# Optimization experiments

Hardware: AMD Instinct MI355X
Metric: run time of the kernel (lower is better)

The kernel has to match this reference:

```python
import jax, jax.numpy as jnp
import numpy as np

N = 8192
TEMP = 0.5
EPS = 1e-12


def _normalize(z):
    # F.normalize(z, p=2, dim=1): x / max(||x||, eps)
    n = jnp.sqrt(jnp.sum(z * z, axis=1, keepdims=True))
    return z / jnp.maximum(n, EPS)


def _gcn(edge_index, edge_weight, x, w, b):
    # torch.sparse.mm(adj, x @ w): out[row] += adj[row, col] * support[col]
    support = x @ w
    msg = support[edge_index[1]] * edge_weight[:, None]
    return jax.ops.segment_sum(msg, edge_index[0], num_segments=N) + b


def _encoder(edge_index, edge_weight, feat, w_l1a, b_l1a, w_l1b, b_l1b, w_g1, b_g1, w_g2, b_g2):
    x = jax.nn.relu(feat @ w_l1a + b_l1a) @ w_l1b + b_l1b  # [N, 32]
    h = jax.nn.relu(_gcn(edge_index, edge_weight, x, w_g1, b_g1))  # [N, hid]
    return _gcn(edge_index, edge_weight, h, w_g2, b_g2)  # [N, act_fn]


def _proj(h, w_fc1, b_fc1, w_fc2, b_fc2):
    return jax.nn.elu(h @ w_fc1 + b_fc1) @ w_fc2 + b_fc2


def _loss(z1, z2):
    z1n = _normalize(z1)
    z2n = _normalize(z2)
    refl = jnp.exp((z1n @ z1n.T) / TEMP)      # [N, N]
    between = jnp.exp((z1n @ z2n.T) / TEMP)   # [N, N]
    denom = refl.sum(1) + between.sum(1) - jnp.diagonal(refl)
    return -jnp.log(jnp.diagonal(between) / denom)


def setup_inputs() -> dict:
    key = jax.random.key(0)
    ks = jax.random.split(key, 20)
    E = 262144
    in_dim, hid_dim, act_fn, out_dim = 512, 256, 128, 64

    def kaiming(k, shape):
        fan_in = shape[0]
        bound = np.sqrt(6.0 / fan_in)
        return jax.random.uniform(k, shape, jnp.float32, -bound, bound)

    return {
        "feat1": jax.random.normal(ks[0], (N, in_dim), jnp.float32),
        "feat2": jax.random.normal(ks[1], (N, in_dim), jnp.float32),
        "edge_index1": jax.random.randint(ks[2], (2, E), 0, N, jnp.int32),
        "edge_weight1": jax.random.uniform(ks[3], (E,), jnp.float32),
        "edge_index2": jax.random.randint(ks[4], (2, E), 0, N, jnp.int32),
        "edge_weight2": jax.random.uniform(ks[5], (E,), jnp.float32),
        "w_l1a": kaiming(ks[6], (in_dim, 64)),
        "b_l1a": jnp.zeros((64,), jnp.float32),
        "w_l1b": kaiming(ks[7], (64, 32)),
        "b_l1b": jnp.zeros((32,), jnp.float32),
        "w_g1": kaiming(ks[8], (32, hid_dim)),
        "b_g1": jnp.zeros((hid_dim,), jnp.float32),
        "w_g2": kaiming(ks[9], (hid_dim, act_fn)),
        "b_g2": jnp.zeros((act_fn,), jnp.float32),
        "w_fc1": kaiming(ks[10], (act_fn, out_dim)),
        "b_fc1": jnp.zeros((out_dim,), jnp.float32),
        "w_fc2": kaiming(ks[11], (out_dim, act_fn)),
        "b_fc2": jnp.zeros((act_fn,), jnp.float32),
    }


def reference(feat1, feat2, edge_index1, edge_weight1, edge_index2, edge_weight2,
              w_l1a, b_l1a, w_l1b, b_l1b, w_g1, b_g1, w_g2, b_g2,
              w_fc1, b_fc1, w_fc2, b_fc2):
    h1 = _encoder(edge_index1, edge_weight1, feat1, w_l1a, b_l1a, w_l1b, b_l1b, w_g1, b_g1, w_g2, b_g2)
    h2 = _encoder(edge_index2, edge_weight2, feat2, w_l1a, b_l1a, w_l1b, b_l1b, w_g1, b_g1, w_g2, b_g2)
    z1 = _proj(h1, w_fc1, b_fc1, w_fc2, b_fc2)
    z2 = _proj(h2, w_fc1, b_fc1, w_fc2, b_fc2)
    l1 = _loss(z1, z2)
    l2 = _loss(z2, z1)
    return ((l1 + l2) * 0.5).mean()
```

## Files before the change

kernel.cpp:

```cpp
#include <hip/hip_runtime.h>
#include <hip/hip_bf16.h>
#include <math.h>


#define NROWS 8192
#define MROWS 16384
#define NEDGE 262144

typedef __attribute__((ext_vector_type(8))) short bf16x8;
typedef __attribute__((ext_vector_type(4))) float f32x4;
typedef __attribute__((ext_vector_type(2))) float f32x2;
typedef long long i64;

__device__ __forceinline__ short f2bf(float f){
  union { float f; unsigned u; } cv; cv.f = f;
  unsigned u = cv.u;
  unsigned r = (u + 0x7fffu + ((u >> 16) & 1u)) >> 16;
  return (short)r;
}
__device__ __forceinline__ f32x4 mfma16(bf16x8 a, bf16x8 b, f32x4 c){
  return __builtin_amdgcn_mfma_f32_16x16x32_bf16(a, b, c, 0, 0, 0);
}
__device__ __forceinline__ float fexp2(float x){
#if __has_builtin(__builtin_amdgcn_exp2f)
  return __builtin_amdgcn_exp2f(x);
#else
  return exp2f(x);
#endif
}

__device__ unsigned char f2e4m3_sw(float f){
  float a = fabsf(f);
  unsigned s = (__float_as_uint(f)>>24)&0x80u;
  if (!(a>0.f)) return (unsigned char)s;
  if (a>448.f) a=448.f;
  int e; frexpf(a,&e);
  int eff=e-1;
  unsigned code;
  if (eff<-6){
    float q=rintf(a*512.f);
    code=(unsigned)q; if(code>7)code=7;
  } else {
    float q=rintf(a*exp2f((float)(3-eff)));
    unsigned mant=(unsigned)q;
    if(mant>=16){mant=8;eff++;}
    if(eff>8) return (unsigned char)(s|0x7e);
    code=((unsigned)(eff+7)<<3)|(mant-8);
  }
  return (unsigned char)(s|code);
}
__device__ __forceinline__ unsigned short pack2fp8(float a, float b){
#if __has_builtin(__builtin_amdgcn_cvt_pk_fp8_f32)
  int v = __builtin_amdgcn_cvt_pk_fp8_f32(a, b, 0, false);
  return (unsigned short)(v & 0xffff);
#else
  return (unsigned short)((unsigned)f2e4m3_sw(a) | ((unsigned)f2e4m3_sw(b)<<8));
#endif
}

struct WtArgs {
  const float* src[6];
  short* dst[6];
  int K[6], N[6];
  int off[7];
  int nwt;
};
__global__ void setup_k(WtArgs a, const int* __restrict__ ei1, const int* __restrict__ ei2,
                        int* __restrict__ deg1, int* __restrict__ deg2){
  int b = blockIdx.x;
  if (b < a.nwt){
    int i = b*256 + threadIdx.x;
    if (i >= a.off[6]) return;
    int s = 0;
    #pragma unroll
    for (int j=1;j<6;j++) if (i >= a.off[j]) s=j;
    int l = i - a.off[s];
    int K=a.K[s], N=a.N[s];
    int k=l/N, n=l-k*N;
    a.dst[s][(long)n*K+k] = f2bf(a.src[s][l]);
  } else {
    int hb = b - a.nwt;
    const int* ei = (hb < NEDGE/256) ? ei1 : ei2;
    int* deg = (hb < NEDGE/256) ? deg1 : deg2;
    int e = (hb % (NEDGE/256))*256 + threadIdx.x;
    atomicAdd(&deg[ei[e]], 1);
  }
}

__global__ __launch_bounds__(256) void mlp12_k(const float* __restrict__ F0, const float* __restrict__ F1,
                                               const short* __restrict__ Wa, const float* __restrict__ ba,
                                               const short* __restrict__ Wb, const float* __restrict__ bb,
                                               short* __restrict__ xb){
  __shared__ short As[32*520];
  __shared__ short a1s[32*72];
  const int tid = threadIdx.x;
  const int m0 = blockIdx.x*32;
  const float* F = (m0 < NROWS) ? (F0 + (long)m0*512) : (F1 + (long)(m0-NROWS)*512);
  {
    float4 st[16];
    #pragma unroll
    for (int i=0;i<16;i++) st[i] = *(const float4*)(F + (long)(i*256+tid)*4);
    #pragma unroll
    for (int i=0;i<16;i++){
      int idx = i*256+tid, row = idx>>7, c4 = idx&127;
      unsigned lo = (unsigned)(unsigned short)f2bf(st[i].x) | ((unsigned)(unsigned short)f2bf(st[i].y)<<16);
      unsigned hi = (unsigned)(unsigned short)f2bf(st[i].z) | ((unsigned)(unsigned short)f2bf(st[i].w)<<16);
      uint2 o = {lo, hi};
      *(uint2*)&As[row*520 + c4*4] = o;
    }
  }
  __syncthreads();
  const int wave = tid>>6, lane = tid&63, quad = lane>>4, cl = lane&15;
  f32x4 zero = {0.f,0.f,0.f,0.f};
  {
    const int wno = wave*16;
    f32x4 acc[2] = {zero, zero};
    #pragma unroll
    for (int kc=0;kc<16;kc++){
      const int ko = kc*32 + quad*8;
      bf16x8 a0 = *(const bf16x8*)&As[(cl)*520 + ko];
      bf16x8 a1 = *(const bf16x8*)&As[(16+cl)*520 + ko];
      bf16x8 b = *(const bf16x8*)(Wa + (long)(wno + cl)*512 + ko);
      acc[0] = mfma16(a0, b, acc[0]);
      acc[1] = mfma16(a1, b, acc[1]);
    }
    int col = wno + cl;
    float bv = ba[col];
    #pragma unroll
    for (int mt=0;mt<2;mt++)
      #pragma unroll
      for (int r=0;r<4;r++)
        a1s[(mt*16 + quad*4 + r)*72 + col] = f2bf(fmaxf(acc[mt][r] + bv, 0.f));
  }
  __syncthreads();
  if (wave < 2){
    f32x4 acc2[2] = {zero, zero};
    #pragma unroll
    for (int kc=0;kc<2;kc++){
      const int ko = kc*32 + quad*8;
      bf16x8 a = *(const bf16x8*)&a1s[(wave*16+cl)*72 + ko];
      #pragma unroll
      for (int nt=0;nt<2;nt++){
        bf16x8 b = *(const bf16x8*)(Wb + (long)(nt*16 + cl)*64 + ko);
        acc2[nt] = mfma16(a, b, acc2[nt]);
      }
    }
    #pragma unroll
    for (int nt=0;nt<2;nt++){
      int col = nt*16 + cl;
      float bv = bb[col];
      #pragma unroll
      for (int r=0;r<4;r++)
        xb[(long)(m0 + wave*16 + quad*4 + r)*32 + col] = f2bf(acc2[nt][r] + bv);
    }
  }
}

__global__ void scan2_k(const int* __restrict__ deg1, int* __restrict__ rs1, int* __restrict__ cur1,
                        const int* __restrict__ deg2, int* __restrict__ rs2, int* __restrict__ cur2){
  const int* deg = blockIdx.x ? deg2 : deg1;
  int* rowstart = blockIdx.x ? rs2 : rs1;
  int* cursor = blockIdx.x ? cur2 : cur1;
  __shared__ int csum[256];
  int t = threadIdx.x;
  int loc[32];
  int s = 0;
  for (int j=0;j<32;j++){ int d = deg[t*32+j]; loc[j] = s; s += d; }
  int v = s;
  csum[t] = v;
  __syncthreads();
  for (int st=1; st<256; st<<=1){
    int o = (t >= st) ? csum[t-st] : 0;
    __syncthreads();
    v += o;
    csum[t] = v;
    __syncthreads();
  }
  int base = v - s;
  for (int j=0;j<32;j++){ int w = base + loc[j]; rowstart[t*32+j]=w; cursor[t*32+j]=w; }
  if (t==255) rowstart[NROWS] = v;
}
__global__ void fill2_k(const int* __restrict__ ei1, const float* __restrict__ w1, int* __restrict__ cur1,
                        int* __restrict__ ecol1, float* __restrict__ ew1,
                        const int* __restrict__ ei2, const float* __restrict__ w2, int* __restrict__ cur2,
                        int* __restrict__ ecol2, float* __restrict__ ew2){
  int b = blockIdx.x;
  bool g2 = (b >= NEDGE/256);
  const int* ei = g2 ? ei2 : ei1;
  const float* w = g2 ? w2 : w1;
  int* cursor = g2 ? cur2 : cur1;
  int* ecol = g2 ? ecol2 : ecol1;
  float* ew = g2 ? ew2 : ew1;
  int e = (b % (NEDGE/256))*256 + threadIdx.x;
  int r = ei[e];
  int p = atomicAdd(&cursor[r], 1);
  ecol[p] = ei[NEDGE + e];
  ew[p] = w[e];
}

__device__ __forceinline__ void acc8(float* acc, int4 v, float f){
  const unsigned* u = (const unsigned*)&v;
  #pragma unroll
  for (int i=0;i<4;i++){
    union{unsigned x; float y;} lo, hi;
    lo.x = u[i] << 16;
    hi.x = u[i] & 0xffff0000u;
    acc[2*i]   = fmaf(f, lo.y, acc[2*i]);
    acc[2*i+1] = fmaf(f, hi.y, acc[2*i+1]);
  }
}
template<int C>
__device__ __forceinline__ void gather_row(float* acc, const short* sb,
                                           const int* ec, const float* w, int s, int e){
  int k = s;
  for (; k+16 <= e; k+=16){
    int c[16]; float f[16]; int4 v[16];
    #pragma unroll
    for (int u=0;u<16;u++){ c[u]=ec[k+u]; f[u]=w[k+u]; }
    #pragma unroll
    for (int u=0;u<16;u++) v[u] = *(const int4*)(sb + (long)c[u]*C);
    #pragma unroll
    for (int u=0;u<16;u++) acc8(acc, v[u], f[u]);
  }
  for (; k+4 <= e; k+=4){
    int c0=ec[k],c1=ec[k+1],c2=ec[k+2],c3=ec[k+3];
    float f0=w[k],f1=w[k+1],f2=w[k+2],f3=w[k+3];
    int4 v0 = *(const int4*)(sb + (long)c0*C);
    int4 v1 = *(const int4*)(sb + (long)c1*C);
    int4 v2 = *(const int4*)(sb + (long)c2*C);
    int4 v3 = *(const int4*)(sb + (long)c3*C);
    acc8(acc,v0,f0); acc8(acc,v1,f1); acc8(acc,v2,f2); acc8(acc,v3,f3);
  }
  for (; k < e; k++){
    int4 v0 = *(const int4*)(sb + (long)ec[k]*C);
    acc8(acc,v0,w[k]);
  }
}

template<int C, bool RELU, bool HASB>
__global__ __launch_bounds__(256) void gather_k(const short* __restrict__ sup,
    const int* __restrict__ rs1, const int* __restrict__ ec1, const float* __restrict__ w1,
    const int* __restrict__ rs2, const int* __restrict__ ec2, const float* __restrict__ w2,
    const float* __restrict__ bias, short* __restrict__ out){
  constexpr int G = C/8;
  const int g = threadIdx.x % G;
  const int sub = threadIdx.x / G;
  const int row = blockIdx.x*(256/G) + sub;
  const int* rs; const int* ec; const float* w; int soff, lr;
  if (row < NROWS){ rs=rs1; ec=ec1; w=w1; soff=0; lr=row; }
  else            { rs=rs2; ec=ec2; w=w2; soff=NROWS; lr=row-NROWS; }
  const short* sb = sup + (long)soff*C + g*8;
  float acc[8];
  #pragma unroll
  for (int j=0;j<8;j++) acc[j] = HASB ? bias[g*8+j] : 0.f;
  gather_row<C>(acc, sb, ec, w, rs[lr], rs[lr+1]);
  int4 ov;
  unsigned* ou = (unsigned*)&ov;
  #pragma unroll
  for (int i=0;i<4;i++){
    float a0 = acc[2*i], a1 = acc[2*i+1];
    if (RELU){ a0 = fmaxf(a0,0.f); a1 = fmaxf(a1,0.f); }
    ou[i] = (unsigned)(unsigned short)f2bf(a0) | ((unsigned)(unsigned short)f2bf(a1)<<16);
  }
  *(int4*)(out + (long)row*C + g*8) = ov;
}

__global__ __launch_bounds__(256) void gg_k(const short* __restrict__ xb,
    const int* __restrict__ rs1, const int* __restrict__ ec1, const float* __restrict__ w1,
    const int* __restrict__ rs2, const int* __restrict__ ec2, const float* __restrict__ w2,
    const short* __restrict__ Wg1, const float* __restrict__ bg1,
    const short* __restrict__ Wg2, short* __restrict__ s2){
  __shared__ short axs[64*40];
  __shared__ short hbs[64*264];
  const int tid = threadIdx.x;
  const int m0 = blockIdx.x*64;
  {
    const int g = tid & 3, sub = tid >> 2;
    const int row = m0 + sub;
    const int* rs; const int* ec; const float* w; int soff, lr;
    if (row < NROWS){ rs=rs1; ec=ec1; w=w1; soff=0; lr=row; }
    else            { rs=rs2; ec=ec2; w=w2; soff=NROWS; lr=row-NROWS; }
    const short* sb = xb + (long)soff*32 + g*8;
    float acc[8];
    #pragma unroll
    for (int j=0;j<8;j++) acc[j] = 0.f;
    gather_row<32>(acc, sb, ec, w, rs[lr], rs[lr+1]);
    int4 ov;
    unsigned* ou = (unsigned*)&ov;
    #pragma unroll
    for (int i=0;i<4;i++)
      ou[i] = (unsigned)(unsigned short)f2bf(acc[2*i]) | ((unsigned)(unsigned short)f2bf(acc[2*i+1])<<16);
    *(int4*)&axs[sub*40 + g*8] = ov;
  }
  __syncthreads();
  const int wave = tid>>6, lane = tid&63, quad = lane>>4, cl = lane&15;
  f32x4 zero = {0.f,0.f,0.f,0.f};
  {
    const int wno = wave*64;
    f32x4 acc[4][4];
    #pragma unroll
    for (int i=0;i<4;i++)
      #pragma unroll
      for (int j=0;j<4;j++) acc[i][j]=zero;
    const int ko = quad*8;
    bf16x8 a[4], b[4];
    #pragma unroll
    for (int mt=0;mt<4;mt++)
      a[mt] = *(const bf16x8*)&axs[(mt*16+cl)*40 + ko];
    #pragma unroll
    for (int nt=0;nt<4;nt++)
      b[nt] = *(const bf16x8*)(Wg1 + (long)(wno + nt*16 + cl)*32 + ko);
    #pragma unroll
    for (int mt=0;mt<4;mt++)
      #pragma unroll
      for (int nt=0;nt<4;nt++)
        acc[mt][nt] = mfma16(a[mt], b[nt], acc[mt][nt]);
    #pragma unroll
    for (int nt=0;nt<4;nt++){
      int col = wno + nt*16 + cl;
      float bv = bg1[col];
      #pragma unroll
      for (int mt=0;mt<4;mt++)
        #pragma unroll
        for (int r=0;r<4;r++)
          hbs[(mt*16 + quad*4 + r)*264 + col] = f2bf(fmaxf(acc[mt][nt][r] + bv, 0.f));
    }
  }
  __syncthreads();
  {
    const int wno = wave*32;
    f32x4 acc[4][2];
    #pragma unroll
    for (int i=0;i<4;i++){ acc[i][0]=zero; acc[i][1]=zero; }
    #pragma unroll
    for (int kc=0;kc<8;kc++){
      const int ko = kc*32 + quad*8;
      bf16x8 a[4], b[2];
      #pragma unroll
      for (int mt=0;mt<4;mt++)
        a[mt] = *(const bf16x8*)&hbs[(mt*16+cl)*264 + ko];
      #pragma unroll
      for (int nt=0;nt<2;nt++)
        b[nt] = *(const bf16x8*)(Wg2 + (long)(wno + nt*16 + cl)*256 + ko);
      #pragma unroll
      for (int mt=0;mt<4;mt++)
        #pragma unroll
        for (int nt=0;nt<2;nt++)
          acc[mt][nt] = mfma16(a[mt], b[nt], acc[mt][nt]);
    }
    #pragma unroll
    for (int mt=0;mt<4;mt++)
      #pragma unroll
      for (int nt=0;nt<2;nt++){
        int col = wno + nt*16 + cl;
        #pragma unroll
        for (int r=0;r<4;r++)
          s2[(long)(m0 + mt*16 + quad*4 + r)*128 + col] = f2bf(acc[mt][nt][r]);
      }
  }
}

__global__ __launch_bounds__(256) void pn_k(const short* __restrict__ hh,
    const short* __restrict__ Wf1, const float* __restrict__ bf1,
    const short* __restrict__ Wf2, const float* __restrict__ bf2,
    unsigned short* __restrict__ Zf, float* __restrict__ bdot){
  __shared__ short hs[64*136];
  __shared__ short t2s[64*72];
  __shared__ float zs[64*132];
  __shared__ float sp[4][64];
  __shared__ float dp[4][32];
  __shared__ float rnS[64];
  const float SQKE = 1.6986436f;
  const int tid = threadIdx.x;
  const int wave = tid>>6, lane = tid&63, quad = lane>>4, cl = lane&15;
  const int m0h = blockIdx.x*32;
  {
    const short* r1 = hh + (long)m0h*128;
    const short* r2 = hh + (long)(NROWS + m0h)*128;
    #pragma unroll
    for (int i=0;i<2;i++){
      int idx = i*256 + tid;
      int row = idx >> 4, c16 = idx & 15;
      *(int4*)&hs[row*136 + c16*8] = *(const int4*)(r1 + row*128 + c16*8);
      *(int4*)&hs[(32+row)*136 + c16*8] = *(const int4*)(r2 + row*128 + c16*8);
    }
  }
  __syncthreads();
  f32x4 zero = {0.f,0.f,0.f,0.f};
  {
    const int wno = wave*16;
    f32x4 acc[4];
    #pragma unroll
    for (int i=0;i<4;i++) acc[i]=zero;
    #pragma unroll
    for (int kc=0;kc<4;kc++){
      const int ko = kc*32 + quad*8;
      bf16x8 a[4], b;
      #pragma unroll
      for (int mt=0;mt<4;mt++)
        a[mt] = *(const bf16x8*)&hs[(mt*16+cl)*136 + ko];
      b = *(const bf16x8*)(Wf1 + (long)(wno + cl)*128 + ko);
      #pragma unroll
      for (int mt=0;mt<4;mt++) acc[mt] = mfma16(a[mt], b, acc[mt]);
    }
    int col = wno + cl;
    float bv = bf1[col];
    #pragma unroll
    for (int mt=0;mt<4;mt++)
      #pragma unroll
      for (int r=0;r<4;r++){
        float v = acc[mt][r] + bv;
        v = (v > 0.f) ? v : expm1f(v);
        t2s[(mt*16 + quad*4 + r)*72 + col] = f2bf(v);
      }
  }
  __syncthreads();
  {
    const int wno = wave*32;
    f32x4 acc[4][2];
    #pragma unroll
    for (int i=0;i<4;i++){ acc[i][0]=zero; acc[i][1]=zero; }
    #pragma unroll
    for (int kc=0;kc<2;kc++){
      const int ko = kc*32 + quad*8;
      bf16x8 a[4], b[2];
      #pragma unroll
      for (int mt=0;mt<4;mt++)
        a[mt] = *(const bf16x8*)&t2s[(mt*16+cl)*72 + ko];
      #pragma unroll
      for (int nt=0;nt<2;nt++)
        b[nt] = *(const bf16x8*)(Wf2 + (long)(wno + nt*16 + cl)*64 + ko);
      #pragma unroll
      for (int mt=0;mt<4;mt++)
        #pragma unroll
        for (int nt=0;nt<2;nt++)
          acc[mt][nt] = mfma16(a[mt], b[nt], acc[mt][nt]);
    }
    #pragma unroll
    for (int mt=0;mt<4;mt++)
      #pragma unroll
      for (int nt=0;nt<2;nt++){
        int col = wno + nt*16 + cl;
        float bv = bf2[col];
        #pragma unroll
        for (int r=0;r<4;r++)
          zs[(mt*16 + quad*4 + r)*132 + col] = acc[mt][nt][r] + bv;
      }
  }
  __syncthreads();
  {
    int row = tid & 63, qtr = tid >> 6;
    const float* zr = &zs[row*132 + qtr*32];
    float s = 0.f;
    #pragma unroll 8
    for (int c=0;c<32;c++) s += zr[c]*zr[c];
    sp[qtr][row] = s;
    if (row < 32){
      const float* zb_ = &zs[(row+32)*132 + qtr*32];
      float d = 0.f;
      #pragma unroll 8
      for (int c=0;c<32;c++) d += zr[c]*zb_[c];
      dp[qtr][row] = d;
    }
  }
  __syncthreads();
  if (tid < 64){
    float ssq = sp[0][tid]+sp[1][tid]+sp[2][tid]+sp[3][tid];
    rnS[tid] = 1.f / fmaxf(sqrtf(ssq), 1e-12f);
  }
  __syncthreads();
  if (tid < 32){
    float dot = dp[0][tid]+dp[1][tid]+dp[2][tid]+dp[3][tid];
    bdot[m0h + tid] = dot * rnS[tid] * rnS[tid+32];
  }
  {
    int lr = tid >> 2;
    int grow = (lr < 32) ? (m0h + lr) : (NROWS + m0h + lr - 32);
    float s = rnS[lr] * SQKE;
    int p0 = (tid & 3)*16;
    #pragma unroll
    for (int pp=0;pp<16;pp++){
      int p = p0 + pp;
      int d = p>>1, h = p&1, kc = d>>3, q = (d>>1)&3, j4 = d&1;
      long o = ((long)(grow>>4)*512 + kc*128 + j4 + ((grow&15)+16*q)*2)*2 + h;
      Zf[o] = pack2fp8(zs[lr*132 + 2*p]*s, zs[lr*132 + 2*p + 1]*s);
    }
  }
}

__global__ __launch_bounds__(256,4) void gram3_k(const unsigned char* __restrict__ Zf,
                                                 float* __restrict__ P){
  __shared__ float srow[4][64];
  __shared__ float scol[4][64];
  const int wave = threadIdx.x>>6, lane = threadIdx.x&63;
  const int t = blockIdx.x*4 + wave;
  int ti = (int)((513.0f - sqrtf(513.0f*513.0f - 8.0f*(float)t))*0.5f);
  while ((ti+1)*256 - ((ti+1)*ti)/2 <= t) ti++;
  while (ti*256 - (ti*(ti-1))/2 > t) ti--;
  const int tj = ti + (t - (ti*256 - (ti*(ti-1))/2));
  const unsigned char* za = Zf + (long)ti*16*512 + lane*8;
  const unsigned char* zb = Zf + (long)tj*16*512 + lane*8;
  const int quad = lane>>4, cl = lane&15;

  f32x4 zero = {0.f,0.f,0.f,0.f};
  f32x2 z2 = {0.f,0.f};
  f32x2 cs[4] = {z2,z2,z2,z2};

  i64 Bf[4][4];
  #pragma unroll
  for (int nt=0;nt<4;nt++)
    #pragma unroll
    for (int kc=0;kc<4;kc++)
      Bf[nt][kc] = *(const i64*)(zb + (nt*4+kc)*512);

  i64 Ab[2][4];
  #pragma unroll
  for (int kc=0;kc<4;kc++) Ab[0][kc] = *(const i64*)(za + kc*512);
  #pragma unroll
  for (int kc=0;kc<4;kc++) Ab[1][kc] = *(const i64*)(za + (4+kc)*512);

  auto exprow = [&](const f32x4* ar, int mt){
    f32x2 r01 = z2, r23 = z2;
    #pragma unroll
    for (int nt=0;nt<4;nt++){
      f32x4 v = ar[nt];
      float e0 = fexp2(v[0]), e1 = fexp2(v[1]);
      float e2 = fexp2(v[2]), e3 = fexp2(v[3]);
      f32x2 p01 = {e0,e1}, p23 = {e2,e3};
      r01 += p01; r23 += p23;
      cs[nt] += p01; cs[nt] += p23;
    }
    union{f32x2 v; double d;} u0, u1;
    u0.v = r01; u1.v = r23;
    #pragma unroll
    for (int m=1;m<16;m<<=1){
      union{double d; f32x2 v;} o0, o1;
      o0.d = __shfl_xor(u0.d, m); o1.d = __shfl_xor(u1.d, m);
      u0.v += o0.v; u1.v += o1.v;
    }
    if (cl==0){
      f32x4 rv = {u0.v.x, u0.v.y, u1.v.x, u1.v.y};
      *(f32x4*)&srow[wave][mt*16 + quad*4] = rv;
    }
  };

  f32x4 acc2[2][4];
  #pragma unroll
  for (int nt=0;nt<4;nt++){
    f32x4 a = zero;
    #pragma unroll
    for (int kc=0;kc<4;kc++)
      a = __builtin_amdgcn_mfma_f32_16x16x32_fp8_fp8(Ab[0][kc], Bf[nt][kc], a, 0, 0, 0);
    acc2[0][nt] = a;
  }
  #pragma unroll
  for (int mt=1; mt<4; mt++){
    const int cur = mt&1, prv = cur^1;
    if (mt<3){
      #pragma unroll
      for (int kc=0;kc<4;kc++) Ab[prv][kc] = *(const i64*)(za + ((mt+1)*4+kc)*512);
    }
    #pragma unroll
    for (int nt=0;nt<4;nt++){
      f32x4 a = zero;
      #pragma unroll
      for (int kc=0;kc<4;kc++)
        a = __builtin_amdgcn_mfma_f32_16x16x32_fp8_fp8(Ab[cur][kc], Bf[nt][kc], a, 0, 0, 0);
      acc2[cur][nt] = a;
    }
    exprow(&acc2[prv][0], mt-1);
  }
  exprow(&acc2[1][0], 3);

  __threadfence_block();
  P[((long)ti*256 + tj)*64 + lane] = srow[wave][lane];
  if (ti != tj){
    #pragma unroll
    for (int nt=0;nt<4;nt++){
      float s = cs[nt].x + cs[nt].y;
      s += __shfl_xor(s,16); s += __shfl_xor(s,32);
      if (quad==0) scol[wave][nt*16 + cl] = s;
    }
    __threadfence_block();
    P[((long)tj*256 + ti)*64 + lane] = scol[wave][lane];
  }
}

__global__ void rloss_k(const float* __restrict__ P, const float* __restrict__ bdot,
                        float* __restrict__ out){
  __shared__ float red[256];
  const float E2 = 7.3890560989306495f;
  int t = threadIdx.x;
  int i = blockIdx.x*256 + t;
  int j = i + NROWS;
  const float* p1 = P + (long)(i>>6)*256*64 + (i&63);
  const float* p2 = P + (long)(j>>6)*256*64 + (j&63);
  float s1 = 0.f, s2 = 0.f;
  #pragma unroll 8
  for (int b=0;b<256;b++){ s1 += p1[b*64]; s2 += p2[b*64]; }
  float lb = 2.f * bdot[i];
  float term = 0.5f * ((logf(s1 - E2) - lb) + (logf(s2 - E2) - lb));
  red[t]=term; __syncthreads();
  for (int st=128; st>0; st>>=1){ if (t<st) red[t]+=red[t+st]; __syncthreads(); }
  if (t==0) atomicAdd(out, red[0] / (float)NROWS);
}

extern "C" void kernel_launch(void* const* d_in, const int* in_sizes, int n_in,
                              void* d_out, int out_size, void* d_ws, size_t ws_size,
                              hipStream_t stream){
  const float* feat1 = (const float*)d_in[0];
  const float* feat2 = (const float*)d_in[1];
  const int*   ei1   = (const int*)d_in[2];
  const float* w1    = (const float*)d_in[3];
  const int*   ei2   = (const int*)d_in[4];
  const float* w2    = (const float*)d_in[5];
  const float* w_l1a = (const float*)d_in[6];
  const float* b_l1a = (const float*)d_in[7];
  const float* w_l1b = (const float*)d_in[8];
  const float* b_l1b = (const float*)d_in[9];
  const float* w_g1  = (const float*)d_in[10];
  const float* b_g1  = (const float*)d_in[11];
  const float* w_g2  = (const float*)d_in[12];
  const float* b_g2  = (const float*)d_in[13];
  const float* w_fc1 = (const float*)d_in[14];
  const float* b_fc1 = (const float*)d_in[15];
  const float* w_fc2 = (const float*)d_in[16];
  const float* b_fc2 = (const float*)d_in[17];

  float* P = (float*)d_ws;
  char* base = (char*)d_ws;
  size_t off = (size_t)17<<20;
  auto alloc = [&](size_t bytes)->void*{
    void* r = base + off;
    off = (off + bytes + 255) & ~(size_t)255;
    return r;
  };
  short* xb   = (short*)alloc((size_t)MROWS*32*2);
  short* s2   = (short*)alloc((size_t)MROWS*128*2);
  short* hh   = (short*)alloc((size_t)MROWS*128*2);
  short* wl1a_t = (short*)alloc(512*64*2);
  short* wl1b_t = (short*)alloc(64*32*2);
  short* wg1_t  = (short*)alloc(32*256*2);
  short* wg2_t  = (short*)alloc(256*128*2);
  short* wfc1_t = (short*)alloc(128*64*2);
  short* wfc2_t = (short*)alloc(64*128*2);
  unsigned short* Zf = (unsigned short*)alloc((size_t)MROWS*128);
  int*   deg1 = (int*)alloc(NROWS*4);
  int*   deg2 = (int*)alloc(NROWS*4);
  int* rs1  = (int*)alloc((NROWS+1)*4);
  int* cur1 = (int*)alloc(NROWS*4);
  int* rs2  = (int*)alloc((NROWS+1)*4);
  int* cur2 = (int*)alloc(NROWS*4);
  int*   ecol1 = (int*)alloc((size_t)NEDGE*4);
  float* ewt1  = (float*)alloc((size_t)NEDGE*4);
  int*   ecol2 = (int*)alloc((size_t)NEDGE*4);
  float* ewt2  = (float*)alloc((size_t)NEDGE*4);
  float* bdot  = (float*)alloc(NROWS*4);

  hipMemsetAsync(deg1, 0, (size_t)2*NROWS*4, stream);
  hipMemsetAsync(d_out, 0, sizeof(float), stream);

  WtArgs wa;
  wa.src[0]=w_l1a; wa.dst[0]=wl1a_t; wa.K[0]=512; wa.N[0]=64;
  wa.src[1]=w_l1b; wa.dst[1]=wl1b_t; wa.K[1]=64;  wa.N[1]=32;
  wa.src[2]=w_g1;  wa.dst[2]=wg1_t;  wa.K[2]=32;  wa.N[2]=256;
  wa.src[3]=w_g2;  wa.dst[3]=wg2_t;  wa.K[3]=256; wa.N[3]=128;
  wa.src[4]=w_fc1; wa.dst[4]=wfc1_t; wa.K[4]=128; wa.N[4]=64;
  wa.src[5]=w_fc2; wa.dst[5]=wfc2_t; wa.K[5]=64;  wa.N[5]=128;
  wa.off[0]=0;
  for (int i=0;i<6;i++) wa.off[i+1] = wa.off[i] + wa.K[i]*wa.N[i];
  wa.nwt = (wa.off[6]+255)/256;

  setup_k<<<wa.nwt + 2*(NEDGE/256),256,0,stream>>>(wa, ei1, ei2, deg1, deg2);
  scan2_k<<<2,256,0,stream>>>(deg1, rs1, cur1, deg2, rs2, cur2);
  fill2_k<<<2*(NEDGE/256),256,0,stream>>>(ei1, w1, cur1, ecol1, ewt1,
                                          ei2, w2, cur2, ecol2, ewt2);

  mlp12_k<<<MROWS/32,256,0,stream>>>(feat1, feat2, wl1a_t, b_l1a, wl1b_t, b_l1b, xb);
  gg_k<<<MROWS/64,256,0,stream>>>(xb, rs1,ecol1,ewt1, rs2,ecol2,ewt2,
                                  wg1_t, b_g1, wg2_t, s2);
  gather_k<128,false,true><<<MROWS/16,256,0,stream>>>(s2, rs1,ecol1,ewt1,
                                                      rs2,ecol2,ewt2, b_g2, hh);
  pn_k<<<NROWS/32,256,0,stream>>>(hh, wfc1_t, b_fc1, wfc2_t, b_fc2, Zf, bdot);

  gram3_k<<<8224,256,0,stream>>>((const unsigned char*)Zf, P);
  rloss_k<<<NROWS/256,256,0,stream>>>(P, bdot, (float*)d_out);
}
```

Measured before the change: 263.8 us.

## Use gfx950 scaled 16x16x128 FP8 MFMA with repacked fragment layout in gram kernel

Replaces the four chained 16x16x32 FP8 MFMAs per output tile with a single MFMA scale 16x16x128 instruction, using unit scale factors (0x7F). The FP8 normalized-embedding buffer is rewritten into a new layout so each lane loads one contiguous 32-byte fragment per tile instead of four separate 8-byte loads. This is meant to cut MFMA issue count and global load instructions in the exp-sum gram kernel, and to make the producer's stores simpler. It depends on the new packing matching the K-ordering the scaled MFMA expects, which is a correctness risk.

```diff
diff --git a/kernel.cpp b/kernel.cpp
--- a/kernel.cpp
+++ b/kernel.cpp
@@ -10,6 +10,7 @@
 typedef __attribute__((ext_vector_type(8))) short bf16x8;
 typedef __attribute__((ext_vector_type(4))) float f32x4;
 typedef __attribute__((ext_vector_type(2))) float f32x2;
+typedef __attribute__((ext_vector_type(8))) int i32x8;
 typedef long long i64;
 
 __device__ __forceinline__ short f2bf(float f){
@@ -478,12 +479,11 @@
     int grow = (lr < 32) ? (m0h + lr) : (NROWS + m0h + lr - 32);
     float s = rnS[lr] * SQKE;
     int p0 = (tid & 3)*16;
+    long gbase = (long)(grow>>4)*1024 + (long)(grow&15)*16 + (long)(p0>>4)*256;
     #pragma unroll
     for (int pp=0;pp<16;pp++){
       int p = p0 + pp;
-      int d = p>>1, h = p&1, kc = d>>3, q = (d>>1)&3, j4 = d&1;
-      long o = ((long)(grow>>4)*512 + kc*128 + j4 + ((grow&15)+16*q)*2)*2 + h;
-      Zf[o] = pack2fp8(zs[lr*132 + 2*p]*s, zs[lr*132 + 2*p + 1]*s);
+      Zf[gbase + pp] = pack2fp8(zs[lr*132 + 2*p]*s, zs[lr*132 + 2*p + 1]*s);
     }
   }
 }
@@ -498,26 +498,22 @@
   while ((ti+1)*256 - ((ti+1)*ti)/2 <= t) ti++;
   while (ti*256 - (ti*(ti-1))/2 > t) ti--;
   const int tj = ti + (t - (ti*256 - (ti*(ti-1))/2));
-  const unsigned char* za = Zf + (long)ti*16*512 + lane*8;
-  const unsigned char* zb = Zf + (long)tj*16*512 + lane*8;
+  const unsigned char* za = Zf + (long)ti*8192 + lane*32;
+  const unsigned char* zb = Zf + (long)tj*8192 + lane*32;
   const int quad = lane>>4, cl = lane&15;
 
   f32x4 zero = {0.f,0.f,0.f,0.f};
   f32x2 z2 = {0.f,0.f};
   f32x2 cs[4] = {z2,z2,z2,z2};
 
-  i64 Bf[4][4];
+  i32x8 Bf[4];
   #pragma unroll
   for (int nt=0;nt<4;nt++)
-    #pragma unroll
-    for (int kc=0;kc<4;kc++)
-      Bf[nt][kc] = *(const i64*)(zb + (nt*4+kc)*512);
-
-  i64 Ab[2][4];
-  #pragma unroll
-  for (int kc=0;kc<4;kc++) Ab[0][kc] = *(const i64*)(za + kc*512);
-  #pragma unroll
-  for (int kc=0;kc<4;kc++) Ab[1][kc] = *(const i64*)(za + (4+kc)*512);
+    Bf[nt] = *(const i32x8*)(zb + nt*2048);
+
+  i32x8 Ab[2];
+  Ab[0] = *(const i32x8*)(za);
+  Ab[1] = *(const i32x8*)(za + 2048);
 
   auto exprow = [&](const f32x4* ar, int mt){
     f32x2 r01 = z2, r23 = z2;
@@ -544,30 +540,21 @@
     }
   };
 
+  const int SC1 = 0x7F;
   f32x4 acc2[2][4];
   #pragma unroll
-  for (int nt=0;nt<4;nt++){
-    f32x4 a = zero;
-    #pragma unroll
-    for (int kc=0;kc<4;kc++)
-      a = __builtin_amdgcn_mfma_f32_16x16x32_fp8_fp8(Ab[0][kc], Bf[nt][kc], a, 0, 0, 0);
-    acc2[0][nt] = a;
-  }
+  for (int nt=0;nt<4;nt++)
+    acc2[0][nt] = __builtin_amdgcn_mfma_scale_f32_16x16x128_f8f6f4(
+        Ab[0], Bf[nt], zero, 0, 0, 0, SC1, 0, SC1);
   #pragma unroll
   for (int mt=1; mt<4; mt++){
     const int cur = mt&1, prv = cur^1;
-    if (mt<3){
-      #pragma unroll
-      for (int kc=0;kc<4;kc++) Ab[prv][kc] = *(const i64*)(za + ((mt+1)*4+kc)*512);
-    }
-    #pragma unroll
-    for (int nt=0;nt<4;nt++){
-      f32x4 a = zero;
-      #pragma unroll
-      for (int kc=0;kc<4;kc++)
-        a = __builtin_amdgcn_mfma_f32_16x16x32_fp8_fp8(Ab[cur][kc], Bf[nt][kc], a, 0, 0, 0);
-      acc2[cur][nt] = a;
-    }
+    if (mt<3)
+      Ab[prv] = *(const i32x8*)(za + (mt+1)*2048);
+    #pragma unroll
+    for (int nt=0;nt<4;nt++)
+      acc2[cur][nt] = __builtin_amdgcn_mfma_scale_f32_16x16x128_f8f6f4(
+          Ab[cur], Bf[nt], zero, 0, 0, 0, SC1, 0, SC1);
     exprow(&acc2[prv][0], mt-1);
   }
   exprow(&acc2[1][0], 3);
```

Result: no change. 260.5 us (-1.2%).
